# Kernel tuning notes

Measured on AMD Instinct MI355X. Metric: run time of the kernel, lower is better.

The kernel has to match this reference:

```python
import jax, jax.numpy as jnp
import numpy as np

R_MAX = 6.0
P = 6.0
QQ = 14.399645 * 0.5  # metal units, * 0.5


def setup_inputs() -> dict:
    key = jax.random.key(0)
    k1, k2, k3, k4 = jax.random.split(key, 4)
    n_atoms = 100_000
    n_edges = 6_400_000
    num_types = 4
    # atomic numbers for H, C, O, Cu
    Z = jnp.asarray([1.0, 6.0, 8.0, 29.0], dtype=jnp.float32)
    # edge lengths in (0.1, 7.3) so some edges exceed r_max and get cut off
    r = jax.random.uniform(k1, (n_edges,), dtype=jnp.float32) * 7.2 + 0.1
    per_atom_energy = jax.random.normal(k2, (n_atoms, 1), dtype=jnp.float32)
    atom_types = jax.random.randint(k3, (n_atoms,), 0, num_types, dtype=jnp.int64)
    edge_index = jax.random.randint(k4, (2, n_edges), 0, n_atoms, dtype=jnp.int64)
    return {"Z": Z, "r": r, "per_atom_energy": per_atom_energy,
            "atom_types": atom_types, "edge_index": edge_index}


def _zbl_edge_energy(Z, r, atom_types, edge_index):
    pzbl = 0.23
    a0 = 0.4685
    c1, c2, c3, c4 = 0.02817, 0.28022, 0.50986, 0.18175
    d1, d2, d3, d4 = -0.20162, -0.4029, -0.94229, -3.1998
    edge_types = atom_types[edge_index]          # (2, E)
    Zpair = Z[edge_types]                        # (2, E)
    Zi, Zj = Zpair[0], Zpair[1]
    x = (jnp.power(Zi, pzbl) + jnp.power(Zj, pzbl)) * r / a0
    psi = (c1 * jnp.exp(d1 * x) + c2 * jnp.exp(d2 * x)
           + c3 * jnp.exp(d3 * x) + c4 * jnp.exp(d4 * x))
    eng = QQ * (Zi * Zj / r) * psi
    rr = r / R_MAX
    p = P
    cutoff = (1.0 - (p + 1.0) * (p + 2.0) / 2.0 * jnp.power(rr, p)
              + p * (p + 2.0) * jnp.power(rr, p + 1.0)
              - p * (p + 1.0) / 2.0 * jnp.power(rr, p + 2.0))
    cutoff = cutoff * (rr < 1.0).astype(cutoff.dtype)
    return cutoff * eng                          # (E,)


def reference(Z, r, per_atom_energy, atom_types, edge_index):
    edge_eng = _zbl_edge_energy(Z, r, atom_types, edge_index)
    n_atoms = per_atom_energy.shape[0]
    atomic_eng = jax.ops.segment_sum(edge_eng, edge_index[0],
                                     num_segments=n_atoms)[:, None]
    return atomic_eng + per_atom_energy
```

## Files before the change

### kernel.cpp

```cpp
#include <hip/hip_runtime.h>


namespace {
constexpr float PZBL     = 0.23f;
constexpr float A0_INV   = 1.0f / 0.4685f;
constexpr float C1 = 0.02817f, C2 = 0.28022f, C3 = 0.50986f, C4 = 0.18175f;
constexpr float D1 = -0.20162f, D2 = -0.4029f, D3 = -0.94229f, D4 = -3.1998f;
constexpr float QQ       = 14.399645f * 0.5f;
constexpr float RMAX     = 6.0f;
constexpr float RMAX_INV = 1.0f / 6.0f;
constexpr int   TPW_MAX  = 6400;
constexpr int   P1_BLOCK = 256;
constexpr int   P1_GRID  = 1536;
constexpr int   CHUNK2   = 33344;
constexpr int   BLOCK    = 1024;
constexpr int   CHUNK1   = 25600;
constexpr int   S1_MAX   = 64;
}

__global__ void zbl_pack_types(const int* __restrict__ types,
                               unsigned* __restrict__ tpw,
                               int n_words, int n_atoms) {
    int w = blockIdx.x * blockDim.x + threadIdx.x;
    if (w >= n_words) return;
    unsigned v = 0;
    int base = w * 16;
    int m = min(16, n_atoms - base);
    for (int j = 0; j < m; ++j)
        v |= ((unsigned)types[base + j] & 3u) << (2 * j);
    tpw[w] = v;
}

__device__ __forceinline__ float edge_eng_lds(float rk, int ia, int ib,
                                              const unsigned* s_tp,
                                              const float* s_zz,
                                              const float* s_zx) {
    unsigned ti = (s_tp[ia >> 4] >> ((ia & 15) * 2)) & 3u;
    unsigned tj = (s_tp[ib >> 4] >> ((ib & 15) * 2)) & 3u;
    int tp = (int)((ti << 2) | tj);
    float x = s_zx[tp] * rk;
    float psi = C1 * __expf(D1 * x) + C2 * __expf(D2 * x)
              + C3 * __expf(D3 * x) + C4 * __expf(D4 * x);
    float eng = s_zz[tp] * psi * __builtin_amdgcn_rcpf(rk);
    float rr = rk * RMAX_INV;
    float rr2 = rr * rr;
    float rr3 = rr2 * rr;
    float rr6 = rr3 * rr3;
    float cutoff = 1.0f + rr6 * (-28.0f + rr * (48.0f - 21.0f * rr));
    return (rk < RMAX) ? cutoff * eng : 0.0f;
}

__device__ __forceinline__ unsigned pack_rec(int dest, float e) {
    unsigned b = __float_as_uint(e);
    unsigned v = (b + 0x8000u) >> 16;
    return ((unsigned)dest << 15) | (v & 0x7FFFu);
}

__global__ __launch_bounds__(P1_BLOCK) void zbl_energy_kernel(
    const float*    __restrict__ Z,
    const float*    __restrict__ r,
    const int*      __restrict__ ei0,
    const int*      __restrict__ ei1,
    const unsigned* __restrict__ tpw,
    unsigned*       __restrict__ rec,
    int n_tp_words, int n_oct, int n_edges) {
    __shared__ unsigned s_tp[TPW_MAX];
    __shared__ float    s_zz[16];
    __shared__ float    s_zx[16];

    const int tid = threadIdx.x;
    for (int i = tid; i < n_tp_words; i += P1_BLOCK) s_tp[i] = tpw[i];
    if (tid < 16) {
        int ti = tid >> 2, tj = tid & 3;
        float zi = Z[ti], zj = Z[tj];
        s_zz[tid] = QQ * zi * zj;
        s_zx[tid] = (powf(zi, PZBL) + powf(zj, PZBL)) * A0_INV;
    }
    __syncthreads();

    const float4* r4 = (const float4*)r;
    const int4*   a4 = (const int4*)ei0;
    const int4*   b4 = (const int4*)ei1;
    uint4*        rc4 = (uint4*)rec;
    const int stride = gridDim.x * P1_BLOCK;
    const int gtid = blockIdx.x * P1_BLOCK + tid;

    for (int o = gtid; o < n_oct; o += stride) {
        int qa = 2 * o, qb = 2 * o + 1;
        float4 rva = r4[qa], rvb = r4[qb];
        int4   ava = a4[qa], avb = a4[qb];
        int4   bva = b4[qa], bvb = b4[qb];
        uint4 wa, wb;
        wa.x = pack_rec(ava.x, edge_eng_lds(rva.x, ava.x, bva.x, s_tp, s_zz, s_zx));
        wa.y = pack_rec(ava.y, edge_eng_lds(rva.y, ava.y, bva.y, s_tp, s_zz, s_zx));
        wa.z = pack_rec(ava.z, edge_eng_lds(rva.z, ava.z, bva.z, s_tp, s_zz, s_zx));
        wa.w = pack_rec(ava.w, edge_eng_lds(rva.w, ava.w, bva.w, s_tp, s_zz, s_zx));
        wb.x = pack_rec(avb.x, edge_eng_lds(rvb.x, avb.x, bvb.x, s_tp, s_zz, s_zx));
        wb.y = pack_rec(avb.y, edge_eng_lds(rvb.y, avb.y, bvb.y, s_tp, s_zz, s_zx));
        wb.z = pack_rec(avb.z, edge_eng_lds(rvb.z, avb.z, bvb.z, s_tp, s_zz, s_zx));
        wb.w = pack_rec(avb.w, edge_eng_lds(rvb.w, avb.w, bvb.w, s_tp, s_zz, s_zx));
        rc4[qa] = wa;
        rc4[qb] = wb;
    }
    for (int e = 8 * n_oct + gtid; e < n_edges; e += stride) {
        int ia = ei0[e];
        rec[e] = pack_rec(ia, edge_eng_lds(r[e], ia, ei1[e], s_tp, s_zz, s_zx));
    }
}

__global__ __launch_bounds__(BLOCK) void zbl_bin_kernel(
    const uint4* __restrict__ rec4,
    const unsigned* __restrict__ rec,
    float*       __restrict__ partials,
    int n_chunks, int u4_per_slice, int n_u4, int n_records) {
    __shared__ float bins[CHUNK2];
    for (int i = threadIdx.x; i < CHUNK2; i += BLOCK) bins[i] = 0.0f;
    __syncthreads();

    const int c = blockIdx.x % n_chunks;
    const int s = blockIdx.x / n_chunks;
    const unsigned base = (unsigned)c * CHUNK2;

    auto lane = [&](unsigned w) {
        unsigned d = (w >> 15) - base;
        unsigned v = w & 0x7FFFu;
        if (d < (unsigned)CHUNK2 && v != 0u)
            atomicAdd(&bins[d], __uint_as_float(v << 16));
    };

    const int q0 = s * u4_per_slice;
    const int q1 = min(n_u4, q0 + u4_per_slice);
    const uint4 dead = make_uint4(0, 0, 0, 0);

    for (int q = q0 + threadIdx.x; q < q1; q += 2 * BLOCK) {
        uint4 p0 = rec4[q];
        uint4 p1 = (q + BLOCK < q1) ? rec4[q + BLOCK] : dead;
        lane(p0.x); lane(p0.y); lane(p0.z); lane(p0.w);
        lane(p1.x); lane(p1.y); lane(p1.z); lane(p1.w);
    }
    if (s == 0) {
        for (int e = 4 * n_u4 + threadIdx.x; e < n_records; e += BLOCK)
            lane(rec[e]);
    }
    __syncthreads();

    float* dst = partials + (size_t)blockIdx.x * CHUNK2;
    for (int i = threadIdx.x; i < CHUNK2; i += BLOCK) dst[i] = bins[i];
}

__global__ void zbl_reduce_out(const float* __restrict__ pae,
                               const float* __restrict__ partials,
                               float* __restrict__ out,
                               int n_atoms, int n_chunks, int n_slices,
                               int chunk) {
    int a = blockIdx.x * blockDim.x + threadIdx.x;
    if (a >= n_atoms) return;
    int c = a / chunk;
    int i = a - c * chunk;
    const float* p = partials + (size_t)c * chunk + i;
    const size_t stride = (size_t)n_chunks * chunk;
    float s0 = 0.0f, s1 = 0.0f, s2 = 0.0f, s3 = 0.0f;
    int s = 0;
    for (; s + 4 <= n_slices; s += 4) {
        s0 += p[(size_t)(s + 0) * stride];
        s1 += p[(size_t)(s + 1) * stride];
        s2 += p[(size_t)(s + 2) * stride];
        s3 += p[(size_t)(s + 3) * stride];
    }
    for (; s < n_slices; ++s) s0 += p[(size_t)s * stride];
    out[a] = pae[a] + ((s0 + s1) + (s2 + s3));
}

__global__ __launch_bounds__(BLOCK) void zbl_chunk_kernel(
    const float*    __restrict__ Z,
    const float*    __restrict__ r,
    const int*      __restrict__ ei0,
    const int*      __restrict__ ei1,
    const unsigned* __restrict__ tpw,
    float*          __restrict__ partials,
    int n_chunks, int n_tp_words, int quads_per_slice,
    int n_quads, int n_edges) {
    __shared__ float    bins[CHUNK1];
    __shared__ unsigned s_tp[TPW_MAX];
    __shared__ float    s_zz[16];
    __shared__ float    s_zx[16];
    const int tid = threadIdx.x;
    for (int i = tid; i < n_tp_words; i += BLOCK) s_tp[i] = tpw[i];
    if (tid < 16) {
        int ti = tid >> 2, tj = tid & 3;
        float zi = Z[ti], zj = Z[tj];
        s_zz[tid] = QQ * zi * zj;
        s_zx[tid] = (powf(zi, PZBL) + powf(zj, PZBL)) * A0_INV;
    }
    for (int i = tid; i < CHUNK1; i += BLOCK) bins[i] = 0.0f;
    __syncthreads();
    const int c = blockIdx.x % n_chunks;
    const int s = blockIdx.x / n_chunks;
    const int base = c * CHUNK1;
    const int q0 = s * quads_per_slice;
    const int q1 = min(n_quads, q0 + quads_per_slice);
    for (int q = q0 + tid; q < q1; q += BLOCK) {
        int4 av = ((const int4*)ei0)[q];
        unsigned d0 = (unsigned)(av.x - base);
        unsigned d1 = (unsigned)(av.y - base);
        unsigned d2 = (unsigned)(av.z - base);
        unsigned d3 = (unsigned)(av.w - base);
        bool m0 = d0 < (unsigned)CHUNK1, m1 = d1 < (unsigned)CHUNK1;
        bool m2 = d2 < (unsigned)CHUNK1, m3 = d3 < (unsigned)CHUNK1;
        if (!(m0 | m1 | m2 | m3)) continue;
        float4 rv = ((const float4*)r)[q];
        int4   bv = ((const int4*)ei1)[q];
        if (m0) { float e = edge_eng_lds(rv.x, av.x, bv.x, s_tp, s_zz, s_zx);
                  if (e != 0.0f) atomicAdd(&bins[d0], e); }
        if (m1) { float e = edge_eng_lds(rv.y, av.y, bv.y, s_tp, s_zz, s_zx);
                  if (e != 0.0f) atomicAdd(&bins[d1], e); }
        if (m2) { float e = edge_eng_lds(rv.z, av.z, bv.z, s_tp, s_zz, s_zx);
                  if (e != 0.0f) atomicAdd(&bins[d2], e); }
        if (m3) { float e = edge_eng_lds(rv.w, av.w, bv.w, s_tp, s_zz, s_zx);
                  if (e != 0.0f) atomicAdd(&bins[d3], e); }
    }
    if (s == 0) {
        for (int e = 4 * n_quads + tid; e < n_edges; e += BLOCK) {
            int ia = ei0[e];
            unsigned d = (unsigned)(ia - base);
            if (d < (unsigned)CHUNK1) {
                float e2 = edge_eng_lds(r[e], ia, ei1[e], s_tp, s_zz, s_zx);
                if (e2 != 0.0f) atomicAdd(&bins[d], e2);
            }
        }
    }
    __syncthreads();
    float* dst = partials + (size_t)blockIdx.x * CHUNK1;
    for (int i = tid; i < CHUNK1; i += BLOCK) dst[i] = bins[i];
}

__global__ void zbl_init_out(const float* __restrict__ pae,
                             float* __restrict__ out, int n) {
    int i = blockIdx.x * blockDim.x + threadIdx.x;
    if (i < n) out[i] = pae[i];
}

__global__ __launch_bounds__(256) void zbl_edge_fallback(
    const float* __restrict__ Z,
    const float* __restrict__ r,
    const int*   __restrict__ ei0,
    const int*   __restrict__ ei1,
    const int*   __restrict__ types,
    float*       __restrict__ out,
    int n_edges) {
    __shared__ float s_z[4];
    __shared__ float s_zp[4];
    if (threadIdx.x < 4) {
        float z = Z[threadIdx.x];
        s_z[threadIdx.x]  = z;
        s_zp[threadIdx.x] = powf(z, PZBL);
    }
    __syncthreads();
    int e = blockIdx.x * blockDim.x + threadIdx.x;
    if (e >= n_edges) return;
    float rk = r[e];
    if (rk >= RMAX) return;
    int ia = ei0[e], ib = ei1[e];
    int ti = types[ia], tj = types[ib];
    float x = (s_zp[ti] + s_zp[tj]) * rk * A0_INV;
    float psi = C1 * __expf(D1 * x) + C2 * __expf(D2 * x)
              + C3 * __expf(D3 * x) + C4 * __expf(D4 * x);
    float eng = QQ * s_z[ti] * s_z[tj] * psi / rk;
    float rr = rk * RMAX_INV;
    float rr2 = rr * rr, rr3 = rr2 * rr, rr6 = rr3 * rr3;
    float cutoff = 1.0f + rr6 * (-28.0f + rr * (48.0f - 21.0f * rr));
    unsafeAtomicAdd(&out[ia], cutoff * eng);
}

extern "C" void kernel_launch(void* const* d_in, const int* in_sizes, int n_in,
                              void* d_out, int out_size, void* d_ws, size_t ws_size,
                              hipStream_t stream) {
    const float* Z     = (const float*)d_in[0];
    const float* r     = (const float*)d_in[1];
    const float* pae   = (const float*)d_in[2];
    const int*   types = (const int*)d_in[3];
    const int*   ei    = (const int*)d_in[4];

    const int n_edges = in_sizes[1];
    const int n_atoms = in_sizes[2];

    float* out = (float*)d_out;

    const int n_tp_words = (n_atoms + 15) / 16;
    const int n_quads    = (n_edges & 3) ? 0 : (n_edges >> 2);

    const size_t tp_bytes  = ((size_t)n_tp_words * 4 + 15) & ~(size_t)15;
    const size_t rec_bytes = ((size_t)n_edges * 4 + 15) & ~(size_t)15;

    const int nc2 = (n_atoms + CHUNK2 - 1) / CHUNK2;
    int S2 = (nc2 > 0) ? (256 / nc2) : 1;
    while (S2 > 4 &&
           tp_bytes + rec_bytes +
           (size_t)nc2 * S2 * CHUNK2 * sizeof(float) > ws_size) {
        --S2;
    }
    const bool two_phase =
        n_tp_words <= TPW_MAX && n_atoms <= (1 << 17) && S2 >= 4 &&
        n_quads > 0 &&
        tp_bytes + rec_bytes + (size_t)nc2 * S2 * CHUNK2 * sizeof(float)
            <= ws_size;

    const int nc1 = (n_atoms + CHUNK1 - 1) / CHUNK1;
    const bool one_phase =
        n_tp_words <= TPW_MAX &&
        tp_bytes + (size_t)nc1 * S1_MAX * CHUNK1 * sizeof(float) <= ws_size;

    if (two_phase) {
        unsigned* tpw = (unsigned*)d_ws;
        unsigned* rec = (unsigned*)((char*)d_ws + tp_bytes);
        float* partials = (float*)((char*)d_ws + tp_bytes + rec_bytes);

        zbl_pack_types<<<(n_tp_words + 255) / 256, 256, 0, stream>>>(
            types, tpw, n_tp_words, n_atoms);

        const int n_oct = n_quads >> 1;
        zbl_energy_kernel<<<P1_GRID, P1_BLOCK, 0, stream>>>(
            Z, r, ei, ei + n_edges, tpw, rec, n_tp_words, n_oct, n_edges);

        const int n_u4 = n_edges >> 2;
        const int u4_per_slice = (n_u4 + S2 - 1) / S2;
        zbl_bin_kernel<<<nc2 * S2, BLOCK, 0, stream>>>(
            (const uint4*)rec, rec, partials, nc2, u4_per_slice, n_u4, n_edges);

        zbl_reduce_out<<<(n_atoms + 255) / 256, 256, 0, stream>>>(
            pae, partials, out, n_atoms, nc2, S2, CHUNK2);
    } else if (one_phase) {
        unsigned* tpw = (unsigned*)d_ws;
        float* partials = (float*)((char*)d_ws + tp_bytes);

        zbl_pack_types<<<(n_tp_words + 255) / 256, 256, 0, stream>>>(
            types, tpw, n_tp_words, n_atoms);

        const int quads_per_slice = (n_quads + S1_MAX - 1) / S1_MAX;
        zbl_chunk_kernel<<<nc1 * S1_MAX, BLOCK, 0, stream>>>(
            Z, r, ei, ei + n_edges, tpw, partials,
            nc1, n_tp_words, quads_per_slice, n_quads, n_edges);

        zbl_reduce_out<<<(n_atoms + 255) / 256, 256, 0, stream>>>(
            pae, partials, out, n_atoms, nc1, S1_MAX, CHUNK1);
    } else {
        zbl_init_out<<<(n_atoms + 255) / 256, 256, 0, stream>>>(pae, out, n_atoms);
        zbl_edge_fallback<<<(n_edges + 255) / 256, 256, 0, stream>>>(
            Z, r, ei, ei + n_edges, types, out, n_edges);
    }
}
```

Baseline: 163.3 us.

## Bucket edge records by atom chunk with wave ballots to avoid rereads

```diff
diff --git a/kernel.cpp b/kernel.cpp
--- a/kernel.cpp
+++ b/kernel.cpp
@@ -12,6 +12,8 @@
 constexpr int   TPW_MAX  = 6400;
 constexpr int   P1_BLOCK = 256;
 constexpr int   P1_GRID  = 1536;
+constexpr int   P1_WPB   = P1_BLOCK / 64;
+constexpr int   WG_TOTAL = P1_GRID * P1_WPB;
 constexpr int   CHUNK2   = 33344;
 constexpr int   BLOCK    = 1024;
 constexpr int   CHUNK1   = 25600;
@@ -50,20 +52,15 @@
     return (rk < RMAX) ? cutoff * eng : 0.0f;
 }
 
-__device__ __forceinline__ unsigned pack_rec(int dest, float e) {
-    unsigned b = __float_as_uint(e);
-    unsigned v = (b + 0x8000u) >> 16;
-    return ((unsigned)dest << 15) | (v & 0x7FFFu);
-}
-
-__global__ __launch_bounds__(P1_BLOCK) void zbl_energy_kernel(
+__global__ __launch_bounds__(P1_BLOCK) void zbl_energy_bucket(
     const float*    __restrict__ Z,
     const float*    __restrict__ r,
     const int*      __restrict__ ei0,
     const int*      __restrict__ ei1,
     const unsigned* __restrict__ tpw,
     unsigned*       __restrict__ rec,
-    int n_tp_words, int n_oct, int n_edges) {
+    unsigned*       __restrict__ counts,
+    int n_tp_words, int n_quads, int qpw, int cap) {
     __shared__ unsigned s_tp[TPW_MAX];
     __shared__ float    s_zz[16];
     __shared__ float    s_zx[16];
@@ -78,69 +75,90 @@
     }
     __syncthreads();
 
+    const int lane = tid & 63;
+    const int wv   = (blockIdx.x * P1_BLOCK + tid) >> 6;
+    const int q_begin = wv * qpw;
+    const int q_end   = min(n_quads, q_begin + qpw);
+    const unsigned long long lt = (1ull << lane) - 1ull;
+
+    unsigned* seg0 = rec + ((size_t)wv * 3 + 0) * cap;
+    unsigned* seg1 = rec + ((size_t)wv * 3 + 1) * cap;
+    unsigned* seg2 = rec + ((size_t)wv * 3 + 2) * cap;
+    unsigned w0 = 0, w1 = 0, w2 = 0;
+
     const float4* r4 = (const float4*)r;
     const int4*   a4 = (const int4*)ei0;
     const int4*   b4 = (const int4*)ei1;
-    uint4*        rc4 = (uint4*)rec;
-    const int stride = gridDim.x * P1_BLOCK;
-    const int gtid = blockIdx.x * P1_BLOCK + tid;
-
-    for (int o = gtid; o < n_oct; o += stride) {
-        int qa = 2 * o, qb = 2 * o + 1;
-        float4 rva = r4[qa], rvb = r4[qb];
-        int4   ava = a4[qa], avb = a4[qb];
-        int4   bva = b4[qa], bvb = b4[qb];
-        uint4 wa, wb;
-        wa.x = pack_rec(ava.x, edge_eng_lds(rva.x, ava.x, bva.x, s_tp, s_zz, s_zx));
-        wa.y = pack_rec(ava.y, edge_eng_lds(rva.y, ava.y, bva.y, s_tp, s_zz, s_zx));
-        wa.z = pack_rec(ava.z, edge_eng_lds(rva.z, ava.z, bva.z, s_tp, s_zz, s_zx));
-        wa.w = pack_rec(ava.w, edge_eng_lds(rva.w, ava.w, bva.w, s_tp, s_zz, s_zx));
-        wb.x = pack_rec(avb.x, edge_eng_lds(rvb.x, avb.x, bvb.x, s_tp, s_zz, s_zx));
-        wb.y = pack_rec(avb.y, edge_eng_lds(rvb.y, avb.y, bvb.y, s_tp, s_zz, s_zx));
-        wb.z = pack_rec(avb.z, edge_eng_lds(rvb.z, avb.z, bvb.z, s_tp, s_zz, s_zx));
-        wb.w = pack_rec(avb.w, edge_eng_lds(rvb.w, avb.w, bvb.w, s_tp, s_zz, s_zx));
-        rc4[qa] = wa;
-        rc4[qb] = wb;
-    }
-    for (int e = 8 * n_oct + gtid; e < n_edges; e += stride) {
-        int ia = ei0[e];
-        rec[e] = pack_rec(ia, edge_eng_lds(r[e], ia, ei1[e], s_tp, s_zz, s_zx));
-    }
-}
-
-__global__ __launch_bounds__(BLOCK) void zbl_bin_kernel(
-    const uint4* __restrict__ rec4,
+
+    auto emit = [&](int dest, float e, bool lv) {
+        unsigned b   = __float_as_uint(e);
+        unsigned v16 = ((b + 0x4000u) >> 15) & 0xFFFFu;
+        bool valid = lv && (v16 != 0u);
+        unsigned cc = (unsigned)(dest >= CHUNK2) + (unsigned)(dest >= 2 * CHUNK2);
+        unsigned w  = ((unsigned)(dest - (int)cc * CHUNK2) << 16) | v16;
+        unsigned long long m;
+        unsigned n;
+        m = __ballot(valid && cc == 0u);
+        n = (unsigned)__popcll(m);
+        if (n) { if (valid && cc == 0u) seg0[w0 + (unsigned)__popcll(m & lt)] = w;
+                 w0 += n; }
+        m = __ballot(valid && cc == 1u);
+        n = (unsigned)__popcll(m);
+        if (n) { if (valid && cc == 1u) seg1[w1 + (unsigned)__popcll(m & lt)] = w;
+                 w1 += n; }
+        m = __ballot(valid && cc == 2u);
+        n = (unsigned)__popcll(m);
+        if (n) { if (valid && cc == 2u) seg2[w2 + (unsigned)__popcll(m & lt)] = w;
+                 w2 += n; }
+    };
+
+    for (int qb = q_begin; qb < q_end; qb += 128) {
+        int qa = qb + 2 * lane;
+        int ia0 = min(qa,     n_quads - 1);
+        int ia1 = min(qa + 1, n_quads - 1);
+        bool va = qa < q_end;
+        bool vb = (qa + 1) < q_end;
+        float4 rva = r4[ia0], rvb = r4[ia1];
+        int4   ava = a4[ia0], avb = a4[ia1];
+        int4   bva = b4[ia0], bvb = b4[ia1];
+        emit(ava.x, edge_eng_lds(rva.x, ava.x, bva.x, s_tp, s_zz, s_zx), va);
+        emit(ava.y, edge_eng_lds(rva.y, ava.y, bva.y, s_tp, s_zz, s_zx), va);
+        emit(ava.z, edge_eng_lds(rva.z, ava.z, bva.z, s_tp, s_zz, s_zx), va);
+        emit(ava.w, edge_eng_lds(rva.w, ava.w, bva.w, s_tp, s_zz, s_zx), va);
+        emit(avb.x, edge_eng_lds(rvb.x, avb.x, bvb.x, s_tp, s_zz, s_zx), vb);
+        emit(avb.y, edge_eng_lds(rvb.y, avb.y, bvb.y, s_tp, s_zz, s_zx), vb);
+        emit(avb.z, edge_eng_lds(rvb.z, avb.z, bvb.z, s_tp, s_zz, s_zx), vb);
+        emit(avb.w, edge_eng_lds(rvb.w, avb.w, bvb.w, s_tp, s_zz, s_zx), vb);
+    }
+    if (lane == 0) {
+        counts[wv * 3 + 0] = w0;
+        counts[wv * 3 + 1] = w1;
+        counts[wv * 3 + 2] = w2;
+    }
+}
+
+__global__ __launch_bounds__(BLOCK) void zbl_bin_bucket(
     const unsigned* __restrict__ rec,
-    float*       __restrict__ partials,
-    int n_chunks, int u4_per_slice, int n_u4, int n_records) {
+    const unsigned* __restrict__ counts,
+    float*          __restrict__ partials,
+    int n_waves, int cap, int s2) {
     __shared__ float bins[CHUNK2];
     for (int i = threadIdx.x; i < CHUNK2; i += BLOCK) bins[i] = 0.0f;
     __syncthreads();
 
-    const int c = blockIdx.x % n_chunks;
-    const int s = blockIdx.x / n_chunks;
-    const unsigned base = (unsigned)c * CHUNK2;
-
-    auto lane = [&](unsigned w) {
-        unsigned d = (w >> 15) - base;
-        unsigned v = w & 0x7FFFu;
-        if (d < (unsigned)CHUNK2 && v != 0u)
-            atomicAdd(&bins[d], __uint_as_float(v << 16));
-    };
-
-    const int q0 = s * u4_per_slice;
-    const int q1 = min(n_u4, q0 + u4_per_slice);
-    const uint4 dead = make_uint4(0, 0, 0, 0);
-
-    for (int q = q0 + threadIdx.x; q < q1; q += 2 * BLOCK) {
-        uint4 p0 = rec4[q];
-        uint4 p1 = (q + BLOCK < q1) ? rec4[q + BLOCK] : dead;
-        lane(p0.x); lane(p0.y); lane(p0.z); lane(p0.w);
-        lane(p1.x); lane(p1.y); lane(p1.z); lane(p1.w);
-    }
-    if (s == 0) {
-        for (int e = 4 * n_u4 + threadIdx.x; e < n_records; e += BLOCK)
-            lane(rec[e]);
+    const int c    = blockIdx.x % 3;
+    const int s    = blockIdx.x / 3;
+    const int wib  = threadIdx.x >> 6;
+    const int lane = threadIdx.x & 63;
+    const int wstride = s2 * (BLOCK / 64);
+
+    for (int w = s * (BLOCK / 64) + wib; w < n_waves; w += wstride) {
+        unsigned n = counts[w * 3 + c];
+        const unsigned* p = rec + ((size_t)w * 3 + c) * cap;
+        for (unsigned i = (unsigned)lane; i < n; i += 64u) {
+            unsigned x = p[i];
+            atomicAdd(&bins[x >> 16], __uint_as_float((x & 0xFFFFu) << 15));
+        }
     }
     __syncthreads();
 
@@ -289,21 +307,24 @@
     const int n_tp_words = (n_atoms + 15) / 16;
     const int n_quads    = (n_edges & 3) ? 0 : (n_edges >> 2);
 
-    const size_t tp_bytes  = ((size_t)n_tp_words * 4 + 15) & ~(size_t)15;
-    const size_t rec_bytes = ((size_t)n_edges * 4 + 15) & ~(size_t)15;
-
-    const int nc2 = (n_atoms + CHUNK2 - 1) / CHUNK2;
-    int S2 = (nc2 > 0) ? (256 / nc2) : 1;
+    const size_t tp_bytes = ((size_t)n_tp_words * 4 + 15) & ~(size_t)15;
+
+    const int qpw = n_quads > 0 ? (n_quads + WG_TOTAL - 1) / WG_TOTAL : 1;
+    const int cap = 4 * qpw;
+    const size_t cnt_bytes = (((size_t)WG_TOTAL * 3 * 4) + 15) & ~(size_t)15;
+    const size_t rec_bytes = (((size_t)WG_TOTAL * 3 * cap * 4) + 15) & ~(size_t)15;
+
+    int S2 = 256 / 3;
     while (S2 > 4 &&
-           tp_bytes + rec_bytes +
-           (size_t)nc2 * S2 * CHUNK2 * sizeof(float) > ws_size) {
+           tp_bytes + cnt_bytes + rec_bytes +
+           (size_t)3 * S2 * CHUNK2 * sizeof(float) > ws_size) {
         --S2;
     }
     const bool two_phase =
-        n_tp_words <= TPW_MAX && n_atoms <= (1 << 17) && S2 >= 4 &&
-        n_quads > 0 &&
-        tp_bytes + rec_bytes + (size_t)nc2 * S2 * CHUNK2 * sizeof(float)
-            <= ws_size;
+        n_tp_words <= TPW_MAX && n_quads > 0 && S2 >= 4 &&
+        n_atoms <= 3 * CHUNK2 &&
+        tp_bytes + cnt_bytes + rec_bytes +
+            (size_t)3 * S2 * CHUNK2 * sizeof(float) <= ws_size;
 
     const int nc1 = (n_atoms + CHUNK1 - 1) / CHUNK1;
     const bool one_phase =
@@ -311,24 +332,23 @@
         tp_bytes + (size_t)nc1 * S1_MAX * CHUNK1 * sizeof(float) <= ws_size;
 
     if (two_phase) {
-        unsigned* tpw = (unsigned*)d_ws;
-        unsigned* rec = (unsigned*)((char*)d_ws + tp_bytes);
-        float* partials = (float*)((char*)d_ws + tp_bytes + rec_bytes);
+        unsigned* tpw    = (unsigned*)d_ws;
+        unsigned* counts = (unsigned*)((char*)d_ws + tp_bytes);
+        unsigned* rec    = (unsigned*)((char*)d_ws + tp_bytes + cnt_bytes);
+        float* partials  = (float*)((char*)d_ws + tp_bytes + cnt_bytes + rec_bytes);
 
         zbl_pack_types<<<(n_tp_words + 255) / 256, 256, 0, stream>>>(
             types, tpw, n_tp_words, n_atoms);
 
-        const int n_oct = n_quads >> 1;
-        zbl_energy_kernel<<<P1_GRID, P1_BLOCK, 0, stream>>>(
-            Z, r, ei, ei + n_edges, tpw, rec, n_tp_words, n_oct, n_edges);
-
-        const int n_u4 = n_edges >> 2;
-        const int u4_per_slice = (n_u4 + S2 - 1) / S2;
-        zbl_bin_kernel<<<nc2 * S2, BLOCK, 0, stream>>>(
-            (const uint4*)rec, rec, partials, nc2, u4_per_slice, n_u4, n_edges);
+        zbl_energy_bucket<<<P1_GRID, P1_BLOCK, 0, stream>>>(
+            Z, r, ei, ei + n_edges, tpw, rec, counts,
+            n_tp_words, n_quads, qpw, cap);
+
+        zbl_bin_bucket<<<3 * S2, BLOCK, 0, stream>>>(
+            rec, counts, partials, WG_TOTAL, cap, S2);
 
         zbl_reduce_out<<<(n_atoms + 255) / 256, 256, 0, stream>>>(
-            pae, partials, out, n_atoms, nc2, S2, CHUNK2);
+            pae, partials, out, n_atoms, 3, S2, CHUNK2);
     } else if (one_phase) {
         unsigned* tpw = (unsigned*)d_ws;
         float* partials = (float*)((char*)d_ws + tp_bytes);
```

Result: slower. 179.7 us (+10.1%).
